# Optimization experiments

Measured on AMD Instinct MI355X. Metric: run time of the kernel, lower is better.

The kernel has to match this reference:

```python
import jax, jax.numpy as jnp
import numpy as np

B, SQ, SK, D, UNITS = 4, 2048, 2048, 1024, 1024

def setup_inputs() -> dict:
    key = jax.random.key(0)
    ks = jax.random.split(key, 5)
    scale = 1.0 / np.sqrt(D)
    return {
        "q": jax.random.normal(ks[0], (B, SQ, D), dtype=jnp.float32),
        "k": jax.random.normal(ks[1], (B, SK, D), dtype=jnp.float32),
        "v": jax.random.normal(ks[2], (B, SK, D), dtype=jnp.float32),
        "W1_w": jax.random.normal(ks[3], (D, UNITS), dtype=jnp.float32) * scale,
        "W1_b": jnp.zeros((UNITS,), dtype=jnp.float32),
        "W2_w": jax.random.normal(ks[4], (D, UNITS), dtype=jnp.float32) * scale,
        "W2_b": jnp.zeros((UNITS,), dtype=jnp.float32),
    }

def reference(q, k, v, W1_w, W1_b, W2_w, W2_b):
    # Dense projections (keras Dense: x @ W + b)
    l1 = q @ W1_w + W1_b            # [B, Sq, units]
    l2 = k @ W2_w + W2_b            # [B, Sk, units]
    # score = l1 @ l2^T, scaled by sqrt(score.shape[2]) == sqrt(Sk) (as in original)
    inv_scale = 1.0 / np.sqrt(k.shape[1]).astype(np.float32)
    score = jnp.einsum('bqu,bku->bqk', l1, l2) * inv_scale  # [B, Sq, Sk]
    dist = jax.nn.softmax(score, axis=-1)
    att = jnp.einsum('bqk,bkd->bqd', dist, v)               # [B, Sq, d_v]
    return att
```

## Files before the change

### kernel.cpp

```cpp
#include <hip/hip_runtime.h>
#include <cmath>
#include <stdint.h>


typedef short short8 __attribute__((ext_vector_type(8)));
typedef float f32x4 __attribute__((ext_vector_type(4)));
typedef __bf16 bf16x8 __attribute__((ext_vector_type(8)));

typedef __attribute__((address_space(3))) void lds_void;
typedef __attribute__((address_space(1))) void gbl_void;

__device__ __forceinline__ unsigned short f2b(float x) {
    unsigned u = __builtin_bit_cast(unsigned, x);
    u += 0x7fffu + ((u >> 16) & 1u);
    return (unsigned short)(u >> 16);
}

__global__ void prep_kernel(const float* __restrict__ q,
                            const float* __restrict__ k,
                            const float* __restrict__ v,
                            const float* __restrict__ W1,
                            const float* __restrict__ W2,
                            unsigned short* __restrict__ qbf,
                            unsigned short* __restrict__ kbf,
                            unsigned short* __restrict__ vT,
                            unsigned short* __restrict__ W1t,
                            unsigned short* __restrict__ W2t,
                            float* __restrict__ rs) {
    const int bz = blockIdx.z;
    const int t = threadIdx.x;

    if (bz >= 6) {
        const float* in = (bz < 8) ? q : k;
        unsigned short* out = (bz < 8) ? qbf : kbf;
        const long zi = (bz - 6) & 1;
        const long fb = zi * 2048 + blockIdx.y * 64 + blockIdx.x;
        const long i = (fb * 256 + t) * 8;
        float4 a = *(const float4*)(in + i);
        float4 b = *(const float4*)(in + i + 4);
        union { short8 v8; unsigned short u[8]; } r;
        r.u[0] = f2b(a.x); r.u[1] = f2b(a.y); r.u[2] = f2b(a.z); r.u[3] = f2b(a.w);
        r.u[4] = f2b(b.x); r.u[5] = f2b(b.y); r.u[6] = f2b(b.z); r.u[7] = f2b(b.w);
        *(short8*)(out + i) = r.v8;
        return;
    }

    const int tid2 = blockIdx.y * 64 + blockIdx.x;

    if (bz == 4 && tid2 >= 256 && tid2 < 288) {
        if (rs) rs[(tid2 - 256) * 256 + t] = 0.f;
        return;
    }

    __shared__ float tile[64][65];
    const float* in;
    unsigned short* out;
    int R, C;
    if (bz < 4) {
        R = 2048; C = 1024;
        if (tid2 >= 512) return;
        in = v + (long)bz * R * C;
        out = vT + (long)bz * R * C;
    } else {
        R = 1024; C = 1024;
        if (tid2 >= 256) return;
        in = (bz == 4) ? W1 : W2;
        out = (bz == 4) ? W1t : W2t;
    }
    const int rt = (tid2 >> 4) * 64;
    const int ct = (tid2 & 15) * 64;

    {
        const int rr = t >> 2;
        const int cb = (t & 3) * 16;
        const float* src = in + (long)(rt + rr) * C + ct + cb;
#pragma unroll
        for (int u = 0; u < 4; u++) {
            float4 a = *(const float4*)(src + 4 * u);
            tile[rr][cb + 4 * u + 0] = a.x;
            tile[rr][cb + 4 * u + 1] = a.y;
            tile[rr][cb + 4 * u + 2] = a.z;
            tile[rr][cb + 4 * u + 3] = a.w;
        }
    }
    __syncthreads();
    {
        const int cc = t >> 2;
        const int rb = (t & 3) * 16;
        unsigned short* dst = out + (long)(ct + cc) * R + rt + rb;
#pragma unroll
        for (int u = 0; u < 2; u++) {
            union { short8 v8; unsigned short us[8]; } o;
#pragma unroll
            for (int e = 0; e < 8; e++) o.us[e] = f2b(tile[rb + 8 * u + e][cc]);
            *(short8*)(dst + 8 * u) = o.v8;
        }
    }
}

__device__ __forceinline__ void load16_to_lds(const unsigned short* g,
                                              unsigned short* l) {
    __builtin_amdgcn_global_load_lds((gbl_void*)g, (lds_void*)l, 16, 0, 0);
}

template <int MODE>
__global__ __launch_bounds__(512, 4) void gemm256_kernel(
                               const unsigned short* __restrict__ A,
                               const unsigned short* __restrict__ Bt,
                               const float* __restrict__ bias0,
                               const float* __restrict__ bias1,
                               float* __restrict__ rowsum,
                               void* __restrict__ Cout,
                               int M, int N, int K,
                               float scale,
                               long sA, long sB, long sC) {
    __shared__ __align__(16) unsigned short As[256 * 64];
    __shared__ __align__(16) unsigned short Bs[128 * 64];

    int bx, by, bz;
    {
        const int nx = gridDim.x;
        const int Rt = gridDim.y * gridDim.z;
        if ((Rt & 7) == 0) {
            int flat = ((int)blockIdx.z * gridDim.y + blockIdx.y) * nx + blockIdx.x;
            int rpx = Rt >> 3;
            int c = flat & 7;
            int j = flat >> 3;
            bx = j / rpx;
            int yg = c * rpx + (j - bx * rpx);
            bz = yg / gridDim.y;
            by = yg - bz * gridDim.y;
        } else {
            bx = blockIdx.x; by = blockIdx.y; bz = blockIdx.z;
        }
    }

    A  += (long)bz * sA;
    Bt += (long)bz * sB;

    const int t = threadIdx.x;
    const int lane = t & 63;
    const int wave = t >> 6;
    const int wm = wave >> 1, wn = wave & 1;
    const int row0 = by * 256;
    const int col0 = bx * 128;

    const int rS = lane >> 3;
    const int kOffS = ((lane & 7) ^ rS) * 8;
    const unsigned short* gA[4];
    unsigned short* lA[4];
    const unsigned short* gB[2];
    unsigned short* lB[2];
#pragma unroll
    for (int i = 0; i < 4; i++) {
        const int rowl = wave * 32 + i * 8;
        gA[i] = A + (long)(row0 + rowl + rS) * K + kOffS;
        lA[i] = As + rowl * 64;
    }
#pragma unroll
    for (int i = 0; i < 2; i++) {
        const int rowl = wave * 16 + i * 8;
        gB[i] = Bt + (long)(col0 + rowl + rS) * K + kOffS;
        lB[i] = Bs + rowl * 64;
    }

    const int lr = lane & 15;
    const int quad = lane >> 4;
    const int pc0 = (quad ^ (lr & 7)) * 8;
    const int pc1 = ((4 + quad) ^ (lr & 7)) * 8;

    f32x4 acc[4][4];
#pragma unroll
    for (int i = 0; i < 4; i++)
#pragma unroll
        for (int j = 0; j < 4; j++) acc[i][j] = f32x4{0.f, 0.f, 0.f, 0.f};

    for (int k0 = 0; k0 < K; k0 += 64) {
#pragma unroll
        for (int i = 0; i < 4; i++) load16_to_lds(gA[i] + k0, lA[i]);
#pragma unroll
        for (int i = 0; i < 2; i++) load16_to_lds(gB[i] + k0, lB[i]);
        __syncthreads();

#pragma unroll
        for (int ks = 0; ks < 2; ks++) {
            const int pc = ks ? pc1 : pc0;
            bf16x8 a[4], b[4];
#pragma unroll
            for (int i = 0; i < 4; i++) {
                a[i] = __builtin_bit_cast(bf16x8,
                    *(const short8*)(As + (wm * 64 + i * 16 + lr) * 64 + pc));
                b[i] = __builtin_bit_cast(bf16x8,
                    *(const short8*)(Bs + (wn * 64 + i * 16 + lr) * 64 + pc));
            }
#pragma unroll
            for (int i = 0; i < 4; i++)
#pragma unroll
                for (int j = 0; j < 4; j++)
                    acc[i][j] = __builtin_amdgcn_mfma_f32_16x16x32_bf16(
                        a[i], b[j], acc[i][j], 0, 0, 0);
        }
        __syncthreads();
    }

    const long cbase = (long)bz * sC;

    if (MODE == 0) {
        const float* bp = (bz && bias1) ? bias1 : bias0;
#pragma unroll
        for (int j = 0; j < 4; j++) {
            const int gcol = col0 + wn * 64 + j * 16 + lr;
            const float bv = bp[gcol];
#pragma unroll
            for (int i = 0; i < 4; i++) {
                const int growb = row0 + wm * 64 + i * 16 + quad * 4;
#pragma unroll
                for (int r = 0; r < 4; r++) {
                    float val = acc[i][j][r] * scale + bv;
                    ((unsigned short*)Cout)[cbase + (long)(growb + r) * N + gcol] = f2b(val);
                }
            }
        }
    } else if (MODE == 1) {
        float psum[4][4];
#pragma unroll
        for (int i = 0; i < 4; i++)
#pragma unroll
            for (int r = 0; r < 4; r++) psum[i][r] = 0.f;
#pragma unroll
        for (int j = 0; j < 4; j++) {
            const int gcol = col0 + wn * 64 + j * 16 + lr;
#pragma unroll
            for (int i = 0; i < 4; i++) {
                const int growb = row0 + wm * 64 + i * 16 + quad * 4;
#pragma unroll
                for (int r = 0; r < 4; r++) {
                    float e = __expf(acc[i][j][r] * scale);
                    psum[i][r] += e;
                    ((unsigned short*)Cout)[cbase + (long)(growb + r) * N + gcol] = f2b(e);
                }
            }
        }
#pragma unroll
        for (int i = 0; i < 4; i++)
#pragma unroll
            for (int r = 0; r < 4; r++) {
                float s = psum[i][r];
                s += __shfl_xor(s, 1);
                s += __shfl_xor(s, 2);
                s += __shfl_xor(s, 4);
                s += __shfl_xor(s, 8);
                if (lr == 0) {
                    const int grow = row0 + wm * 64 + i * 16 + quad * 4 + r;
                    atomicAdd(rowsum + (long)bz * M + grow, s);
                }
            }
    } else {
#pragma unroll
        for (int i = 0; i < 4; i++) {
            const int growb = row0 + wm * 64 + i * 16 + quad * 4;
#pragma unroll
            for (int r = 0; r < 4; r++) {
                const float inv = 1.0f / rowsum[(long)bz * M + growb + r];
#pragma unroll
                for (int j = 0; j < 4; j++) {
                    const int gcol = col0 + wn * 64 + j * 16 + lr;
                    ((float*)Cout)[cbase + (long)(growb + r) * N + gcol] =
                        acc[i][j][r] * inv;
                }
            }
        }
    }
}

template <int MODE>
__global__ void gemm128_kernel(const unsigned short* __restrict__ A,
                               const unsigned short* __restrict__ Bt,
                               const float* __restrict__ bias0,
                               const float* __restrict__ bias1,
                               float* __restrict__ rowsum,
                               void* __restrict__ Cout,
                               int M, int N, int K,
                               float scale,
                               long sA, long sB, long sC) {
    __shared__ __align__(16) unsigned short As[128 * 64];
    __shared__ __align__(16) unsigned short Bs[128 * 64];

    int bx, by, bz;
    {
        const int nx = gridDim.x;
        const int Rt = gridDim.y * gridDim.z;
        if ((Rt & 7) == 0) {
            int flat = ((int)blockIdx.z * gridDim.y + blockIdx.y) * nx + blockIdx.x;
            int rpx = Rt >> 3;
            int c = flat & 7;
            int j = flat >> 3;
            bx = j / rpx;
            int yg = c * rpx + (j - bx * rpx);
            bz = yg / gridDim.y;
            by = yg - bz * gridDim.y;
        } else {
            bx = blockIdx.x; by = blockIdx.y; bz = blockIdx.z;
        }
    }

    A  += (long)bz * sA;
    Bt += (long)bz * sB;

    const int t = threadIdx.x;
    const int lane = t & 63;
    const int wave = t >> 6;
    const int wm = wave >> 1, wn = wave & 1;
    const int row0 = by * 128;
    const int col0 = bx * 128;

    const int rS = lane >> 3;
    const int kOffS = ((lane & 7) ^ rS) * 8;
    const unsigned short* gA[4];
    const unsigned short* gB[4];
    unsigned short* lA[4];
    unsigned short* lB[4];
#pragma unroll
    for (int i = 0; i < 4; i++) {
        const int rowl = i * 32 + wave * 8 + rS;
        const int ldsrow = i * 32 + wave * 8;
        gA[i] = A  + (long)(row0 + rowl) * K + kOffS;
        gB[i] = Bt + (long)(col0 + rowl) * K + kOffS;
        lA[i] = As + ldsrow * 64;
        lB[i] = Bs + ldsrow * 64;
    }

    const int lr = lane & 15;
    const int quad = lane >> 4;
    const int pc0 = (quad ^ (lr & 7)) * 8;
    const int pc1 = ((4 + quad) ^ (lr & 7)) * 8;

    f32x4 acc[4][4];
#pragma unroll
    for (int i = 0; i < 4; i++)
#pragma unroll
        for (int j = 0; j < 4; j++) acc[i][j] = f32x4{0.f, 0.f, 0.f, 0.f};

    for (int k0 = 0; k0 < K; k0 += 64) {
#pragma unroll
        for (int i = 0; i < 4; i++) {
            load16_to_lds(gA[i] + k0, lA[i]);
            load16_to_lds(gB[i] + k0, lB[i]);
        }
        __syncthreads();

#pragma unroll
        for (int ks = 0; ks < 2; ks++) {
            const int pc = ks ? pc1 : pc0;
            bf16x8 a[4], b[4];
#pragma unroll
            for (int i = 0; i < 4; i++) {
                a[i] = __builtin_bit_cast(bf16x8,
                    *(const short8*)(As + (wm * 64 + i * 16 + lr) * 64 + pc));
                b[i] = __builtin_bit_cast(bf16x8,
                    *(const short8*)(Bs + (wn * 64 + i * 16 + lr) * 64 + pc));
            }
#pragma unroll
            for (int i = 0; i < 4; i++)
#pragma unroll
                for (int j = 0; j < 4; j++)
                    acc[i][j] = __builtin_amdgcn_mfma_f32_16x16x32_bf16(
                        a[i], b[j], acc[i][j], 0, 0, 0);
        }
        __syncthreads();
    }

    const long cbase = (long)bz * sC;

    if (MODE == 0) {
        const float* bp = (bz && bias1) ? bias1 : bias0;
#pragma unroll
        for (int j = 0; j < 4; j++) {
            const int gcol = col0 + wn * 64 + j * 16 + lr;
            const float bv = bp[gcol];
#pragma unroll
            for (int i = 0; i < 4; i++) {
                const int growb = row0 + wm * 64 + i * 16 + quad * 4;
#pragma unroll
                for (int r = 0; r < 4; r++) {
                    float val = acc[i][j][r] * scale + bv;
                    ((unsigned short*)Cout)[cbase + (long)(growb + r) * N + gcol] = f2b(val);
                }
            }
        }
    } else if (MODE == 1) {
        float psum[4][4];
#pragma unroll
        for (int i = 0; i < 4; i++)
#pragma unroll
            for (int r = 0; r < 4; r++) psum[i][r] = 0.f;
#pragma unroll
        for (int j = 0; j < 4; j++) {
            const int gcol = col0 + wn * 64 + j * 16 + lr;
#pragma unroll
            for (int i = 0; i < 4; i++) {
                const int growb = row0 + wm * 64 + i * 16 + quad * 4;
#pragma unroll
                for (int r = 0; r < 4; r++) {
                    float e = __expf(acc[i][j][r] * scale);
                    psum[i][r] += e;
                    ((unsigned short*)Cout)[cbase + (long)(growb + r) * N + gcol] = f2b(e);
                }
            }
        }
#pragma unroll
        for (int i = 0; i < 4; i++)
#pragma unroll
            for (int r = 0; r < 4; r++) {
                float s = psum[i][r];
                s += __shfl_xor(s, 1);
                s += __shfl_xor(s, 2);
                s += __shfl_xor(s, 4);
                s += __shfl_xor(s, 8);
                if (lr == 0) {
                    const int grow = row0 + wm * 64 + i * 16 + quad * 4 + r;
                    atomicAdd(rowsum + (long)bz * M + grow, s);
                }
            }
    } else {
#pragma unroll
        for (int i = 0; i < 4; i++) {
            const int growb = row0 + wm * 64 + i * 16 + quad * 4;
#pragma unroll
            for (int r = 0; r < 4; r++) {
                const float inv = 1.0f / rowsum[(long)bz * M + growb + r];
#pragma unroll
                for (int j = 0; j < 4; j++) {
                    const int gcol = col0 + wn * 64 + j * 16 + lr;
                    ((float*)Cout)[cbase + (long)(growb + r) * N + gcol] =
                        acc[i][j][r] * inv;
                }
            }
        }
    }
}

extern "C" void kernel_launch(void* const* d_in, const int* in_sizes, int n_in,
                              void* d_out, int out_size, void* d_ws, size_t ws_size,
                              hipStream_t stream) {
    const float* q   = (const float*)d_in[0];
    const float* k   = (const float*)d_in[1];
    const float* v   = (const float*)d_in[2];
    const float* W1w = (const float*)d_in[3];
    const float* W1b = (const float*)d_in[4];
    const float* W2w = (const float*)d_in[5];
    const float* W2b = (const float*)d_in[6];
    float* out = (float*)d_out;

    const int B = 4, SQ = 2048, SK = 2048, D = 1024, U = 1024;
    char* ws = (char*)d_ws;
    const size_t MB = 1024 * 1024;
    unsigned short* qbf = (unsigned short*)(ws + 0);
    unsigned short* kbf = (unsigned short*)(ws + 16 * MB);
    unsigned short* vT  = (unsigned short*)(ws + 32 * MB);
    unsigned short* W1t = (unsigned short*)(ws + 48 * MB);
    unsigned short* W2t = (unsigned short*)(ws + 50 * MB);
    unsigned short* l1  = (unsigned short*)(ws + 52 * MB);
    unsigned short* l2  = (unsigned short*)(ws + 68 * MB);
    unsigned short* sc  = (unsigned short*)(ws + 0);

    float* rowsum;
    bool prep_zeroes_rowsum;
    if (ws_size >= 85 * MB) {
        rowsum = (float*)(ws + 84 * MB);
        prep_zeroes_rowsum = true;
    } else {
        rowsum = (float*)(ws + 50 * MB);
        prep_zeroes_rowsum = false;
    }

    prep_kernel<<<dim3(64, 32, 10), 256, 0, stream>>>(
        q, k, v, W1w, W2w, qbf, kbf, vT, W1t, W2t,
        prep_zeroes_rowsum ? rowsum : nullptr);
    gemm256_kernel<0><<<dim3(U / 128, (B * SQ) / 256, 2), 512, 0, stream>>>(
        qbf, W1t, W1b, W2b, nullptr, l1, B * SQ, U, D, 1.0f,
        (long)8 * 1024 * 1024, (long)1024 * 1024, (long)8 * 1024 * 1024);
    if (!prep_zeroes_rowsum)
        hipMemsetAsync(rowsum, 0, (size_t)B * SQ * sizeof(float), stream);
    const float invs = 1.0f / sqrtf((float)SK);
    gemm256_kernel<1><<<dim3(SK / 128, SQ / 256, B), 512, 0, stream>>>(
        l1, l2, nullptr, nullptr, rowsum, sc, SQ, SK, U, invs,
        (long)SQ * U, (long)SK * U, (long)SQ * SK);
    gemm128_kernel<2><<<dim3(D / 128, SQ / 128, B), 256, 0, stream>>>(
        sc, vT, nullptr, nullptr, rowsum, out, SQ, D, SK, 1.0f,
        (long)SQ * SK, (long)D * SK, (long)SQ * D);
}
```

Baseline: 265.5 us.

## Fuse fp32-to-bf16 cast of q and k into projection GEMM A-loads

Removes the separate prep pass that converted q and k to bf16 in workspace. The projection GEMM now reads fp32 q/k directly, converts them with v_cvt_pk_bf16_f32 and writes them into LDS through registers. This saves a full write and re-read of the bf16 copies. In exchange, the A operand no longer uses async global_load_lds, so it costs registers and may expose load latency in the unpipelined k-loop. Dead MODE branches are also pruned from both GEMM templates.

```diff
diff --git a/kernel.cpp b/kernel.cpp
--- a/kernel.cpp
+++ b/kernel.cpp
@@ -6,6 +6,7 @@
 typedef short short8 __attribute__((ext_vector_type(8)));
 typedef float f32x4 __attribute__((ext_vector_type(4)));
 typedef __bf16 bf16x8 __attribute__((ext_vector_type(8)));
+typedef unsigned int u32x4 __attribute__((ext_vector_type(4)));
 
 typedef __attribute__((address_space(3))) void lds_void;
 typedef __attribute__((address_space(1))) void gbl_void;
@@ -16,35 +17,15 @@
     return (unsigned short)(u >> 16);
 }
 
-__global__ void prep_kernel(const float* __restrict__ q,
-                            const float* __restrict__ k,
-                            const float* __restrict__ v,
+__global__ void prep_kernel(const float* __restrict__ v,
                             const float* __restrict__ W1,
                             const float* __restrict__ W2,
-                            unsigned short* __restrict__ qbf,
-                            unsigned short* __restrict__ kbf,
                             unsigned short* __restrict__ vT,
                             unsigned short* __restrict__ W1t,
                             unsigned short* __restrict__ W2t,
                             float* __restrict__ rs) {
     const int bz = blockIdx.z;
     const int t = threadIdx.x;
-
-    if (bz >= 6) {
-        const float* in = (bz < 8) ? q : k;
-        unsigned short* out = (bz < 8) ? qbf : kbf;
-        const long zi = (bz - 6) & 1;
-        const long fb = zi * 2048 + blockIdx.y * 64 + blockIdx.x;
-        const long i = (fb * 256 + t) * 8;
-        float4 a = *(const float4*)(in + i);
-        float4 b = *(const float4*)(in + i + 4);
-        union { short8 v8; unsigned short u[8]; } r;
-        r.u[0] = f2b(a.x); r.u[1] = f2b(a.y); r.u[2] = f2b(a.z); r.u[3] = f2b(a.w);
-        r.u[4] = f2b(b.x); r.u[5] = f2b(b.y); r.u[6] = f2b(b.z); r.u[7] = f2b(b.w);
-        *(short8*)(out + i) = r.v8;
-        return;
-    }
-
     const int tid2 = blockIdx.y * 64 + blockIdx.x;
 
     if (bz == 4 && tid2 >= 256 && tid2 < 288) {
@@ -58,7 +39,6 @@
     int R, C;
     if (bz < 4) {
         R = 2048; C = 1024;
-        if (tid2 >= 512) return;
         in = v + (long)bz * R * C;
         out = vT + (long)bz * R * C;
     } else {
@@ -103,7 +83,7 @@
     __builtin_amdgcn_global_load_lds((gbl_void*)g, (lds_void*)l, 16, 0, 0);
 }
 
-template <int MODE>
+template <int MODE, int CASTA>
 __global__ __launch_bounds__(512, 4) void gemm256_kernel(
                                const unsigned short* __restrict__ A,
                                const unsigned short* __restrict__ Bt,
@@ -113,7 +93,9 @@
                                void* __restrict__ Cout,
                                int M, int N, int K,
                                float scale,
-                               long sA, long sB, long sC) {
+                               long sA, long sB, long sC,
+                               const float* __restrict__ Afq,
+                               const float* __restrict__ Afk) {
     __shared__ __align__(16) unsigned short As[256 * 64];
     __shared__ __align__(16) unsigned short Bs[128 * 64];
 
@@ -135,7 +117,6 @@
         }
     }
 
-    A  += (long)bz * sA;
     Bt += (long)bz * sB;
 
     const int t = threadIdx.x;
@@ -148,14 +129,20 @@
     const int rS = lane >> 3;
     const int kOffS = ((lane & 7) ^ rS) * 8;
     const unsigned short* gA[4];
+    const float* fA[4];
     unsigned short* lA[4];
     const unsigned short* gB[2];
     unsigned short* lB[2];
 #pragma unroll
     for (int i = 0; i < 4; i++) {
         const int rowl = wave * 32 + i * 8;
-        gA[i] = A + (long)(row0 + rowl + rS) * K + kOffS;
         lA[i] = As + rowl * 64;
+        if (CASTA) {
+            const float* Af = bz ? Afk : Afq;
+            fA[i] = Af + (long)(row0 + rowl + rS) * K + kOffS;
+        } else {
+            gA[i] = A + (long)bz * sA + (long)(row0 + rowl + rS) * K + kOffS;
+        }
     }
 #pragma unroll
     for (int i = 0; i < 2; i++) {
@@ -177,9 +164,24 @@
 
     for (int k0 = 0; k0 < K; k0 += 64) {
 #pragma unroll
-        for (int i = 0; i < 4; i++) load16_to_lds(gA[i] + k0, lA[i]);
-#pragma unroll
         for (int i = 0; i < 2; i++) load16_to_lds(gB[i] + k0, lB[i]);
+        if (CASTA) {
+#pragma unroll
+            for (int i = 0; i < 4; i++) {
+                const float* s = fA[i] + k0;
+                float4 x = *(const float4*)(s);
+                float4 y = *(const float4*)(s + 4);
+                unsigned w0, w1, w2, w3;
+                asm("v_cvt_pk_bf16_f32 %0, %1, %2" : "=v"(w0) : "v"(x.x), "v"(x.y));
+                asm("v_cvt_pk_bf16_f32 %0, %1, %2" : "=v"(w1) : "v"(x.z), "v"(x.w));
+                asm("v_cvt_pk_bf16_f32 %0, %1, %2" : "=v"(w2) : "v"(y.x), "v"(y.y));
+                asm("v_cvt_pk_bf16_f32 %0, %1, %2" : "=v"(w3) : "v"(y.z), "v"(y.w));
+                *(u32x4*)(lA[i] + lane * 8) = u32x4{w0, w1, w2, w3};
+            }
+        } else {
+#pragma unroll
+            for (int i = 0; i < 4; i++) load16_to_lds(gA[i] + k0, lA[i]);
+        }
         __syncthreads();
 
 #pragma unroll
@@ -221,7 +223,7 @@
                 }
             }
         }
-    } else if (MODE == 1) {
+    } else {
         float psum[4][4];
 #pragma unroll
         for (int i = 0; i < 4; i++)
@@ -255,21 +257,6 @@
                     atomicAdd(rowsum + (long)bz * M + grow, s);
                 }
             }
-    } else {
-#pragma unroll
-        for (int i = 0; i < 4; i++) {
-            const int growb = row0 + wm * 64 + i * 16 + quad * 4;
-#pragma unroll
-            for (int r = 0; r < 4; r++) {
-                const float inv = 1.0f / rowsum[(long)bz * M + growb + r];
-#pragma unroll
-                for (int j = 0; j < 4; j++) {
-                    const int gcol = col0 + wn * 64 + j * 16 + lr;
-                    ((float*)Cout)[cbase + (long)(growb + r) * N + gcol] =
-                        acc[i][j][r] * inv;
-                }
-            }
-        }
     }
 }
 
@@ -372,57 +359,7 @@
 
     const long cbase = (long)bz * sC;
 
-    if (MODE == 0) {
-        const float* bp = (bz && bias1) ? bias1 : bias0;
-#pragma unroll
-        for (int j = 0; j < 4; j++) {
-            const int gcol = col0 + wn * 64 + j * 16 + lr;
-            const float bv = bp[gcol];
-#pragma unroll
-            for (int i = 0; i < 4; i++) {
-                const int growb = row0 + wm * 64 + i * 16 + quad * 4;
-#pragma unroll
-                for (int r = 0; r < 4; r++) {
-                    float val = acc[i][j][r] * scale + bv;
-                    ((unsigned short*)Cout)[cbase + (long)(growb + r) * N + gcol] = f2b(val);
-                }
-            }
-        }
-    } else if (MODE == 1) {
-        float psum[4][4];
-#pragma unroll
-        for (int i = 0; i < 4; i++)
-#pragma unroll
-            for (int r = 0; r < 4; r++) psum[i][r] = 0.f;
-#pragma unroll
-        for (int j = 0; j < 4; j++) {
-            const int gcol = col0 + wn * 64 + j * 16 + lr;
-#pragma unroll
-            for (int i = 0; i < 4; i++) {
-                const int growb = row0 + wm * 64 + i * 16 + quad * 4;
-#pragma unroll
-                for (int r = 0; r < 4; r++) {
-                    float e = __expf(acc[i][j][r] * scale);
-                    psum[i][r] += e;
-                    ((unsigned short*)Cout)[cbase + (long)(growb + r) * N + gcol] = f2b(e);
-                }
-            }
-        }
-#pragma unroll
-        for (int i = 0; i < 4; i++)
-#pragma unroll
-            for (int r = 0; r < 4; r++) {
-                float s = psum[i][r];
-                s += __shfl_xor(s, 1);
-                s += __shfl_xor(s, 2);
-                s += __shfl_xor(s, 4);
-                s += __shfl_xor(s, 8);
-                if (lr == 0) {
-                    const int grow = row0 + wm * 64 + i * 16 + quad * 4 + r;
-                    atomicAdd(rowsum + (long)bz * M + grow, s);
-                }
-            }
-    } else {
+    if (MODE == 2) {
 #pragma unroll
         for (int i = 0; i < 4; i++) {
             const int growb = row0 + wm * 64 + i * 16 + quad * 4;
@@ -455,8 +392,6 @@
     const int B = 4, SQ = 2048, SK = 2048, D = 1024, U = 1024;
     char* ws = (char*)d_ws;
     const size_t MB = 1024 * 1024;
-    unsigned short* qbf = (unsigned short*)(ws + 0);
-    unsigned short* kbf = (unsigned short*)(ws + 16 * MB);
     unsigned short* vT  = (unsigned short*)(ws + 32 * MB);
     unsigned short* W1t = (unsigned short*)(ws + 48 * MB);
     unsigned short* W2t = (unsigned short*)(ws + 50 * MB);
@@ -474,18 +409,18 @@
         prep_zeroes_rowsum = false;
     }
 
-    prep_kernel<<<dim3(64, 32, 10), 256, 0, stream>>>(
-        q, k, v, W1w, W2w, qbf, kbf, vT, W1t, W2t,
+    prep_kernel<<<dim3(64, 8, 6), 256, 0, stream>>>(
+        v, W1w, W2w, vT, W1t, W2t,
         prep_zeroes_rowsum ? rowsum : nullptr);
-    gemm256_kernel<0><<<dim3(U / 128, (B * SQ) / 256, 2), 512, 0, stream>>>(
-        qbf, W1t, W1b, W2b, nullptr, l1, B * SQ, U, D, 1.0f,
-        (long)8 * 1024 * 1024, (long)1024 * 1024, (long)8 * 1024 * 1024);
+    gemm256_kernel<0, 1><<<dim3(U / 128, (B * SQ) / 256, 2), 512, 0, stream>>>(
+        nullptr, W1t, W1b, W2b, nullptr, l1, B * SQ, U, D, 1.0f,
+        0, (long)1024 * 1024, (long)8 * 1024 * 1024, q, k);
     if (!prep_zeroes_rowsum)
         hipMemsetAsync(rowsum, 0, (size_t)B * SQ * sizeof(float), stream);
     const float invs = 1.0f / sqrtf((float)SK);
-    gemm256_kernel<1><<<dim3(SK / 128, SQ / 256, B), 512, 0, stream>>>(
+    gemm256_kernel<1, 0><<<dim3(SK / 128, SQ / 256, B), 512, 0, stream>>>(
         l1, l2, nullptr, nullptr, rowsum, sc, SQ, SK, U, invs,
-        (long)SQ * U, (long)SK * U, (long)SQ * SK);
+        (long)SQ * U, (long)SK * U, (long)SQ * SK, nullptr, nullptr);
     gemm128_kernel<2><<<dim3(D / 128, SQ / 128, B), 256, 0, stream>>>(
         sc, vT, nullptr, nullptr, rowsum, out, SQ, D, SK, 1.0f,
         (long)SQ * SK, (long)D * SK, (long)SQ * D);
```

Result: no change. 261.7 us (-1.4%).

## Fuse prep and three GEMMs into one cooperative persistent kernel with grid syncs

Applied to the files above, without the earlier changes.

Adds a cooperative mega_kernel of 512 blocks of 512 threads. It runs the bf16 casts, the transposes (now converting to bf16 inside LDS), the projection GEMM, the exp-score GEMM and the attention GEMM as phases separated by grid-wide syncs. Each phase is remapped so exactly 512 tiles fill the grid, and the final GEMM uses a new 8-wave 128x128 tile routine. The aim is to remove kernel launch boundaries and tail gaps between stages. In exchange it adds grid-barrier cost, fixes occupancy at the cooperative grid size, and keeps the old multi-kernel path as a fallback.

```diff
diff --git a/kernel.cpp b/kernel.cpp
--- a/kernel.cpp
+++ b/kernel.cpp
@@ -1,7 +1,10 @@
 #include <hip/hip_runtime.h>
+#include <hip/hip_cooperative_groups.h>
 #include <cmath>
 #include <stdint.h>
 
+
+namespace cg = cooperative_groups;
 
 typedef short short8 __attribute__((ext_vector_type(8)));
 typedef float f32x4 __attribute__((ext_vector_type(4)));
@@ -14,6 +17,349 @@
     unsigned u = __builtin_bit_cast(unsigned, x);
     u += 0x7fffu + ((u >> 16) & 1u);
     return (unsigned short)(u >> 16);
+}
+
+__device__ __forceinline__ void load16_to_lds(const unsigned short* g,
+                                              unsigned short* l) {
+    __builtin_amdgcn_global_load_lds((gbl_void*)g, (lds_void*)l, 16, 0, 0);
+}
+
+template <int MODE>
+__device__ __forceinline__ void gemm256_phase(
+        unsigned short* As, unsigned short* Bs,
+        const unsigned short* A, const unsigned short* Bt,
+        const float* bias0, const float* bias1,
+        float* rowsum, void* Cout,
+        int M, int N, int K, float scale,
+        long sA, long sB, long sC,
+        int bx, int by, int bz, int t) {
+    A  += (long)bz * sA;
+    Bt += (long)bz * sB;
+
+    const int lane = t & 63;
+    const int wave = t >> 6;
+    const int wm = wave >> 1, wn = wave & 1;
+    const int row0 = by * 256;
+    const int col0 = bx * 128;
+
+    const int rS = lane >> 3;
+    const int kOffS = ((lane & 7) ^ rS) * 8;
+    const unsigned short* gA[4];
+    unsigned short* lA[4];
+    const unsigned short* gB[2];
+    unsigned short* lB[2];
+#pragma unroll
+    for (int i = 0; i < 4; i++) {
+        const int rowl = wave * 32 + i * 8;
+        gA[i] = A + (long)(row0 + rowl + rS) * K + kOffS;
+        lA[i] = As + rowl * 64;
+    }
+#pragma unroll
+    for (int i = 0; i < 2; i++) {
+        const int rowl = wave * 16 + i * 8;
+        gB[i] = Bt + (long)(col0 + rowl + rS) * K + kOffS;
+        lB[i] = Bs + rowl * 64;
+    }
+
+    const int lr = lane & 15;
+    const int quad = lane >> 4;
+    const int pc0 = (quad ^ (lr & 7)) * 8;
+    const int pc1 = ((4 + quad) ^ (lr & 7)) * 8;
+
+    f32x4 acc[4][4];
+#pragma unroll
+    for (int i = 0; i < 4; i++)
+#pragma unroll
+        for (int j = 0; j < 4; j++) acc[i][j] = f32x4{0.f, 0.f, 0.f, 0.f};
+
+    for (int k0 = 0; k0 < K; k0 += 64) {
+#pragma unroll
+        for (int i = 0; i < 4; i++) load16_to_lds(gA[i] + k0, lA[i]);
+#pragma unroll
+        for (int i = 0; i < 2; i++) load16_to_lds(gB[i] + k0, lB[i]);
+        __syncthreads();
+
+#pragma unroll
+        for (int ks = 0; ks < 2; ks++) {
+            const int pc = ks ? pc1 : pc0;
+            bf16x8 a[4], b[4];
+#pragma unroll
+            for (int i = 0; i < 4; i++) {
+                a[i] = __builtin_bit_cast(bf16x8,
+                    *(const short8*)(As + (wm * 64 + i * 16 + lr) * 64 + pc));
+                b[i] = __builtin_bit_cast(bf16x8,
+                    *(const short8*)(Bs + (wn * 64 + i * 16 + lr) * 64 + pc));
+            }
+#pragma unroll
+            for (int i = 0; i < 4; i++)
+#pragma unroll
+                for (int j = 0; j < 4; j++)
+                    acc[i][j] = __builtin_amdgcn_mfma_f32_16x16x32_bf16(
+                        a[i], b[j], acc[i][j], 0, 0, 0);
+        }
+        __syncthreads();
+    }
+
+    const long cbase = (long)bz * sC;
+
+    if (MODE == 0) {
+        const float* bp = (bz && bias1) ? bias1 : bias0;
+#pragma unroll
+        for (int j = 0; j < 4; j++) {
+            const int gcol = col0 + wn * 64 + j * 16 + lr;
+            const float bv = bp[gcol];
+#pragma unroll
+            for (int i = 0; i < 4; i++) {
+                const int growb = row0 + wm * 64 + i * 16 + quad * 4;
+#pragma unroll
+                for (int r = 0; r < 4; r++) {
+                    float val = acc[i][j][r] * scale + bv;
+                    ((unsigned short*)Cout)[cbase + (long)(growb + r) * N + gcol] = f2b(val);
+                }
+            }
+        }
+    } else {
+        float psum[4][4];
+#pragma unroll
+        for (int i = 0; i < 4; i++)
+#pragma unroll
+            for (int r = 0; r < 4; r++) psum[i][r] = 0.f;
+#pragma unroll
+        for (int j = 0; j < 4; j++) {
+            const int gcol = col0 + wn * 64 + j * 16 + lr;
+#pragma unroll
+            for (int i = 0; i < 4; i++) {
+                const int growb = row0 + wm * 64 + i * 16 + quad * 4;
+#pragma unroll
+                for (int r = 0; r < 4; r++) {
+                    float e = __expf(acc[i][j][r] * scale);
+                    psum[i][r] += e;
+                    ((unsigned short*)Cout)[cbase + (long)(growb + r) * N + gcol] = f2b(e);
+                }
+            }
+        }
+#pragma unroll
+        for (int i = 0; i < 4; i++)
+#pragma unroll
+            for (int r = 0; r < 4; r++) {
+                float s = psum[i][r];
+                s += __shfl_xor(s, 1);
+                s += __shfl_xor(s, 2);
+                s += __shfl_xor(s, 4);
+                s += __shfl_xor(s, 8);
+                if (lr == 0) {
+                    const int grow = row0 + wm * 64 + i * 16 + quad * 4 + r;
+                    atomicAdd(rowsum + (long)bz * M + grow, s);
+                }
+            }
+    }
+}
+
+__device__ __forceinline__ void att512_phase(
+        unsigned short* As, unsigned short* Bs,
+        const unsigned short* A, const unsigned short* Bt,
+        const float* rowsum, float* out,
+        int bx, int by, int bz, int t) {
+    const int M = 2048, N = 1024, K = 2048;
+    const long sA = (long)M * K, sB = (long)N * K, sC = (long)M * N;
+    const unsigned short* Ab  = A  + (long)bz * sA;
+    const unsigned short* Btb = Bt + (long)bz * sB;
+
+    const int lane = t & 63;
+    const int w = t >> 6;
+    const int wm = w >> 1, wn = w & 1;
+    const int row0 = by * 128;
+    const int col0 = bx * 128;
+
+    const int rS = lane >> 3;
+    const int kOffS = ((lane & 7) ^ rS) * 8;
+    const unsigned short* gA[2];
+    unsigned short* lA[2];
+    const unsigned short* gB[2];
+    unsigned short* lB[2];
+#pragma unroll
+    for (int i = 0; i < 2; i++) {
+        const int rowl = w * 16 + i * 8;
+        gA[i] = Ab  + (long)(row0 + rowl + rS) * K + kOffS;
+        lA[i] = As + rowl * 64;
+        gB[i] = Btb + (long)(col0 + rowl + rS) * K + kOffS;
+        lB[i] = Bs + rowl * 64;
+    }
+
+    const int lr = lane & 15;
+    const int quad = lane >> 4;
+    const int pc0 = (quad ^ (lr & 7)) * 8;
+    const int pc1 = ((4 + quad) ^ (lr & 7)) * 8;
+
+    f32x4 acc[2][4];
+#pragma unroll
+    for (int i = 0; i < 2; i++)
+#pragma unroll
+        for (int j = 0; j < 4; j++) acc[i][j] = f32x4{0.f, 0.f, 0.f, 0.f};
+
+    for (int k0 = 0; k0 < K; k0 += 64) {
+#pragma unroll
+        for (int i = 0; i < 2; i++) {
+            load16_to_lds(gA[i] + k0, lA[i]);
+            load16_to_lds(gB[i] + k0, lB[i]);
+        }
+        __syncthreads();
+#pragma unroll
+        for (int ks = 0; ks < 2; ks++) {
+            const int pc = ks ? pc1 : pc0;
+            bf16x8 a[2], b[4];
+#pragma unroll
+            for (int i = 0; i < 2; i++)
+                a[i] = __builtin_bit_cast(bf16x8,
+                    *(const short8*)(As + (wm * 32 + i * 16 + lr) * 64 + pc));
+#pragma unroll
+            for (int j = 0; j < 4; j++)
+                b[j] = __builtin_bit_cast(bf16x8,
+                    *(const short8*)(Bs + (wn * 64 + j * 16 + lr) * 64 + pc));
+#pragma unroll
+            for (int i = 0; i < 2; i++)
+#pragma unroll
+                for (int j = 0; j < 4; j++)
+                    acc[i][j] = __builtin_amdgcn_mfma_f32_16x16x32_bf16(
+                        a[i], b[j], acc[i][j], 0, 0, 0);
+        }
+        __syncthreads();
+    }
+
+    const long cbase = (long)bz * sC;
+#pragma unroll
+    for (int i = 0; i < 2; i++) {
+        const int growb = row0 + wm * 32 + i * 16 + quad * 4;
+#pragma unroll
+        for (int r = 0; r < 4; r++) {
+            const float inv = 1.0f / rowsum[(long)bz * M + growb + r];
+#pragma unroll
+            for (int j = 0; j < 4; j++) {
+                const int gcol = col0 + wn * 64 + j * 16 + lr;
+                out[cbase + (long)(growb + r) * N + gcol] = acc[i][j][r] * inv;
+            }
+        }
+    }
+}
+
+struct MegaArgs {
+    const float *q, *k, *v, *W1, *W2, *b1, *b2;
+    unsigned short *qbf, *kbf, *vT, *W1t, *W2t, *l1, *l2, *sc;
+    float *rowsum, *out;
+    float invs;
+};
+
+__global__ __launch_bounds__(512, 4) void mega_kernel(MegaArgs a) {
+    __shared__ __align__(16) unsigned short As[256 * 64];
+    __shared__ __align__(16) unsigned short Bs[128 * 64];
+
+    const int bid = blockIdx.x;
+    const int t = threadIdx.x;
+    const int swz = (bid & 7) * 64 + (bid >> 3);
+
+#pragma unroll
+    for (int it = 0; it < 4; ++it) {
+        const long i = ((long)(it * 512 + bid) * 512 + t) * 8;
+        float4 x = *(const float4*)(a.q + i);
+        float4 y = *(const float4*)(a.q + i + 4);
+        union { short8 v8; unsigned short u[8]; } r;
+        r.u[0] = f2b(x.x); r.u[1] = f2b(x.y); r.u[2] = f2b(x.z); r.u[3] = f2b(x.w);
+        r.u[4] = f2b(y.x); r.u[5] = f2b(y.y); r.u[6] = f2b(y.z); r.u[7] = f2b(y.w);
+        *(short8*)(a.qbf + i) = r.v8;
+    }
+#pragma unroll
+    for (int it = 0; it < 4; ++it) {
+        const long i = ((long)(it * 512 + bid) * 512 + t) * 8;
+        float4 x = *(const float4*)(a.k + i);
+        float4 y = *(const float4*)(a.k + i + 4);
+        union { short8 v8; unsigned short u[8]; } r;
+        r.u[0] = f2b(x.x); r.u[1] = f2b(x.y); r.u[2] = f2b(x.z); r.u[3] = f2b(x.w);
+        r.u[4] = f2b(y.x); r.u[5] = f2b(y.y); r.u[6] = f2b(y.z); r.u[7] = f2b(y.w);
+        *(short8*)(a.kbf + i) = r.v8;
+    }
+    if (bid < 16) a.rowsum[bid * 512 + t] = 0.f;
+
+    {
+        const int half = t >> 8, st = t & 255;
+        unsigned short* tile = As + half * 8192;
+        for (int p = 0; p < 3; ++p) {
+            __syncthreads();
+            const int id = p * 1024 + bid * 2 + half;
+            const float* in = nullptr;
+            unsigned short* outp = nullptr;
+            int R = 0, C = 0, rt = 0, ct = 0;
+            bool active = false;
+            if (id < 2048) {
+                const int batch = id >> 9, ti = id & 511;
+                in = a.v + (long)batch * 2048 * 1024;
+                outp = a.vT + (long)batch * 1024 * 2048;
+                R = 2048; C = 1024;
+                rt = (ti >> 4) * 64; ct = (ti & 15) * 64;
+                active = true;
+            } else {
+                const int wdx = id - 2048;
+                if (wdx < 512) {
+                    in = (wdx < 256) ? a.W1 : a.W2;
+                    outp = (wdx < 256) ? a.W1t : a.W2t;
+                    const int ti = wdx & 255;
+                    R = 1024; C = 1024;
+                    rt = (ti >> 4) * 64; ct = (ti & 15) * 64;
+                    active = true;
+                }
+            }
+            if (active) {
+                const int rr = st >> 2, cb = (st & 3) * 16;
+                const float* src = in + (long)(rt + rr) * C + ct + cb;
+                unsigned short* trow = tile + rr * 65 + cb;
+#pragma unroll
+                for (int u = 0; u < 4; u++) {
+                    float4 x = *(const float4*)(src + 4 * u);
+                    trow[4 * u + 0] = f2b(x.x);
+                    trow[4 * u + 1] = f2b(x.y);
+                    trow[4 * u + 2] = f2b(x.z);
+                    trow[4 * u + 3] = f2b(x.w);
+                }
+            }
+            __syncthreads();
+            if (active) {
+                const int cc = st >> 2, rb = (st & 3) * 16;
+                unsigned short* dst = outp + (long)(ct + cc) * R + rt + rb;
+#pragma unroll
+                for (int u = 0; u < 2; u++) {
+                    union { short8 v8; unsigned short us[8]; } o;
+#pragma unroll
+                    for (int e = 0; e < 8; e++)
+                        o.us[e] = tile[(rb + 8 * u + e) * 65 + cc];
+                    *(short8*)(dst + 8 * u) = o.v8;
+                }
+            }
+        }
+    }
+
+    cg::this_grid().sync();
+
+    {
+        const int bx = swz & 7, by = (swz >> 3) & 31, bz = swz >> 8;
+        gemm256_phase<0>(As, Bs, a.qbf, a.W1t, a.b1, a.b2, nullptr, a.l1,
+                         8192, 1024, 1024, 1.0f,
+                         (long)8 * 1024 * 1024, (long)1024 * 1024,
+                         (long)8 * 1024 * 1024, bx, by, bz, t);
+    }
+    cg::this_grid().sync();
+
+    {
+        const int bx = swz & 15, by = (swz >> 4) & 7, bz = swz >> 7;
+        gemm256_phase<1>(As, Bs, a.l1, a.l2, nullptr, nullptr, a.rowsum, a.sc,
+                         2048, 2048, 1024, a.invs,
+                         (long)2048 * 1024, (long)2048 * 1024,
+                         (long)2048 * 2048, bx, by, bz, t);
+    }
+    cg::this_grid().sync();
+
+    {
+        const int bx = swz & 7, by = (swz >> 3) & 15, bz = swz >> 7;
+        att512_phase(As, Bs, a.sc, a.vT, a.rowsum, a.out, bx, by, bz, t);
+    }
 }
 
 __global__ void prep_kernel(const float* __restrict__ q,
@@ -46,7 +392,6 @@
     }
 
     const int tid2 = blockIdx.y * 64 + blockIdx.x;
-
     if (bz == 4 && tid2 >= 256 && tid2 < 288) {
         if (rs) rs[(tid2 - 256) * 256 + t] = 0.f;
         return;
@@ -69,24 +414,21 @@
     }
     const int rt = (tid2 >> 4) * 64;
     const int ct = (tid2 & 15) * 64;
-
-    {
-        const int rr = t >> 2;
-        const int cb = (t & 3) * 16;
+    {
+        const int rr = t >> 2, cb = (t & 3) * 16;
         const float* src = in + (long)(rt + rr) * C + ct + cb;
 #pragma unroll
         for (int u = 0; u < 4; u++) {
-            float4 a = *(const float4*)(src + 4 * u);
-            tile[rr][cb + 4 * u + 0] = a.x;
-            tile[rr][cb + 4 * u + 1] = a.y;
-            tile[rr][cb + 4 * u + 2] = a.z;
-            tile[rr][cb + 4 * u + 3] = a.w;
+            float4 x = *(const float4*)(src + 4 * u);
+            tile[rr][cb + 4 * u + 0] = x.x;
+            tile[rr][cb + 4 * u + 1] = x.y;
+            tile[rr][cb + 4 * u + 2] = x.z;
+            tile[rr][cb + 4 * u + 3] = x.w;
         }
     }
     __syncthreads();
     {
-        const int cc = t >> 2;
-        const int rb = (t & 3) * 16;
+        const int cc = t >> 2, rb = (t & 3) * 16;
         unsigned short* dst = out + (long)(ct + cc) * R + rt + rb;
 #pragma unroll
         for (int u = 0; u < 2; u++) {
@@ -98,25 +440,16 @@
     }
 }
 
-__device__ __forceinline__ void load16_to_lds(const unsigned short* g,
-                                              unsigned short* l) {
-    __builtin_amdgcn_global_load_lds((gbl_void*)g, (lds_void*)l, 16, 0, 0);
-}
-
 template <int MODE>
 __global__ __launch_bounds__(512, 4) void gemm256_kernel(
-                               const unsigned short* __restrict__ A,
-                               const unsigned short* __restrict__ Bt,
-                               const float* __restrict__ bias0,
-                               const float* __restrict__ bias1,
-                               float* __restrict__ rowsum,
-                               void* __restrict__ Cout,
-                               int M, int N, int K,
-                               float scale,
+                               const unsigned short* A,
+                               const unsigned short* Bt,
+                               const float* bias0, const float* bias1,
+                               float* rowsum, void* Cout,
+                               int M, int N, int K, float scale,
                                long sA, long sB, long sC) {
     __shared__ __align__(16) unsigned short As[256 * 64];
     __shared__ __align__(16) unsigned short Bs[128 * 64];
-
     int bx, by, bz;
     {
         const int nx = gridDim.x;
@@ -134,158 +467,20 @@
             bx = blockIdx.x; by = blockIdx.y; bz = blockIdx.z;
         }
     }
-
-    A  += (long)bz * sA;
-    Bt += (long)bz * sB;
-
-    const int t = threadIdx.x;
-    const int lane = t & 63;
-    const int wave = t >> 6;
-    const int wm = wave >> 1, wn = wave & 1;
-    const int row0 = by * 256;
-    const int col0 = bx * 128;
-
-    const int rS = lane >> 3;
-    const int kOffS = ((lane & 7) ^ rS) * 8;
-    const unsigned short* gA[4];
-    unsigned short* lA[4];
-    const unsigned short* gB[2];
-    unsigned short* lB[2];
-#pragma unroll
-    for (int i = 0; i < 4; i++) {
-        const int rowl = wave * 32 + i * 8;
-        gA[i] = A + (long)(row0 + rowl + rS) * K + kOffS;
-        lA[i] = As + rowl * 64;
-    }
-#pragma unroll
-    for (int i = 0; i < 2; i++) {
-        const int rowl = wave * 16 + i * 8;
-        gB[i] = Bt + (long)(col0 + rowl + rS) * K + kOffS;
-        lB[i] = Bs + rowl * 64;
-    }
-
-    const int lr = lane & 15;
-    const int quad = lane >> 4;
-    const int pc0 = (quad ^ (lr & 7)) * 8;
-    const int pc1 = ((4 + quad) ^ (lr & 7)) * 8;
-
-    f32x4 acc[4][4];
-#pragma unroll
-    for (int i = 0; i < 4; i++)
-#pragma unroll
-        for (int j = 0; j < 4; j++) acc[i][j] = f32x4{0.f, 0.f, 0.f, 0.f};
-
-    for (int k0 = 0; k0 < K; k0 += 64) {
-#pragma unroll
-        for (int i = 0; i < 4; i++) load16_to_lds(gA[i] + k0, lA[i]);
-#pragma unroll
-        for (int i = 0; i < 2; i++) load16_to_lds(gB[i] + k0, lB[i]);
-        __syncthreads();
-
-#pragma unroll
-        for (int ks = 0; ks < 2; ks++) {
-            const int pc = ks ? pc1 : pc0;
-            bf16x8 a[4], b[4];
-#pragma unroll
-            for (int i = 0; i < 4; i++) {
-                a[i] = __builtin_bit_cast(bf16x8,
-                    *(const short8*)(As + (wm * 64 + i * 16 + lr) * 64 + pc));
-                b[i] = __builtin_bit_cast(bf16x8,
-                    *(const short8*)(Bs + (wn * 64 + i * 16 + lr) * 64 + pc));
-            }
-#pragma unroll
-            for (int i = 0; i < 4; i++)
-#pragma unroll
-                for (int j = 0; j < 4; j++)
-                    acc[i][j] = __builtin_amdgcn_mfma_f32_16x16x32_bf16(
-                        a[i], b[j], acc[i][j], 0, 0, 0);
-        }
-        __syncthreads();
-    }
-
-    const long cbase = (long)bz * sC;
-
-    if (MODE == 0) {
-        const float* bp = (bz && bias1) ? bias1 : bias0;
-#pragma unroll
-        for (int j = 0; j < 4; j++) {
-            const int gcol = col0 + wn * 64 + j * 16 + lr;
-            const float bv = bp[gcol];
-#pragma unroll
-            for (int i = 0; i < 4; i++) {
-                const int growb = row0 + wm * 64 + i * 16 + quad * 4;
-#pragma unroll
-                for (int r = 0; r < 4; r++) {
-                    float val = acc[i][j][r] * scale + bv;
-                    ((unsigned short*)Cout)[cbase + (long)(growb + r) * N + gcol] = f2b(val);
-                }
-            }
-        }
-    } else if (MODE == 1) {
-        float psum[4][4];
-#pragma unroll
-        for (int i = 0; i < 4; i++)
-#pragma unroll
-            for (int r = 0; r < 4; r++) psum[i][r] = 0.f;
-#pragma unroll
-        for (int j = 0; j < 4; j++) {
-            const int gcol = col0 + wn * 64 + j * 16 + lr;
-#pragma unroll
-            for (int i = 0; i < 4; i++) {
-                const int growb = row0 + wm * 64 + i * 16 + quad * 4;
-#pragma unroll
-                for (int r = 0; r < 4; r++) {
-                    float e = __expf(acc[i][j][r] * scale);
-                    psum[i][r] += e;
-                    ((unsigned short*)Cout)[cbase + (long)(growb + r) * N + gcol] = f2b(e);
-                }
-            }
-        }
-#pragma unroll
-        for (int i = 0; i < 4; i++)
-#pragma unroll
-            for (int r = 0; r < 4; r++) {
-                float s = psum[i][r];
-                s += __shfl_xor(s, 1);
-                s += __shfl_xor(s, 2);
-                s += __shfl_xor(s, 4);
-                s += __shfl_xor(s, 8);
-                if (lr == 0) {
-                    const int grow = row0 + wm * 64 + i * 16 + quad * 4 + r;
-                    atomicAdd(rowsum + (long)bz * M + grow, s);
-                }
-            }
-    } else {
-#pragma unroll
-        for (int i = 0; i < 4; i++) {
-            const int growb = row0 + wm * 64 + i * 16 + quad * 4;
-#pragma unroll
-            for (int r = 0; r < 4; r++) {
-                const float inv = 1.0f / rowsum[(long)bz * M + growb + r];
-#pragma unroll
-                for (int j = 0; j < 4; j++) {
-                    const int gcol = col0 + wn * 64 + j * 16 + lr;
-                    ((float*)Cout)[cbase + (long)(growb + r) * N + gcol] =
-                        acc[i][j][r] * inv;
-                }
-            }
-        }
-    }
+    gemm256_phase<MODE>(As, Bs, A, Bt, bias0, bias1, rowsum, Cout,
+                        M, N, K, scale, sA, sB, sC, bx, by, bz,
+                        (int)threadIdx.x);
 }
 
 template <int MODE>
 __global__ void gemm128_kernel(const unsigned short* __restrict__ A,
                                const unsigned short* __restrict__ Bt,
-                               const float* __restrict__ bias0,
-                               const float* __restrict__ bias1,
                                float* __restrict__ rowsum,
                                void* __restrict__ Cout,
                                int M, int N, int K,
-                               float scale,
                                long sA, long sB, long sC) {
     __shared__ __align__(16) unsigned short As[128 * 64];
     __shared__ __align__(16) unsigned short Bs[128 * 64];
-
     int bx, by, bz;
     {
         const int nx = gridDim.x;
@@ -306,7 +501,6 @@
 
     A  += (long)bz * sA;
     Bt += (long)bz * sB;
-
     const int t = threadIdx.x;
     const int lane = t & 63;
     const int wave = t >> 6;
@@ -329,7 +523,6 @@
         lA[i] = As + ldsrow * 64;
         lB[i] = Bs + ldsrow * 64;
     }
-
     const int lr = lane & 15;
     const int quad = lane >> 4;
     const int pc0 = (quad ^ (lr & 7)) * 8;
@@ -348,7 +541,6 @@
             load16_to_lds(gB[i] + k0, lB[i]);
         }
         __syncthreads();
-
 #pragma unroll
         for (int ks = 0; ks < 2; ks++) {
             const int pc = ks ? pc1 : pc0;
@@ -371,58 +563,7 @@
     }
 
     const long cbase = (long)bz * sC;
-
-    if (MODE == 0) {
-        const float* bp = (bz && bias1) ? bias1 : bias0;
-#pragma unroll
-        for (int j = 0; j < 4; j++) {
-            const int gcol = col0 + wn * 64 + j * 16 + lr;
-            const float bv = bp[gcol];
-#pragma unroll
-            for (int i = 0; i < 4; i++) {
-                const int growb = row0 + wm * 64 + i * 16 + quad * 4;
-#pragma unroll
-                for (int r = 0; r < 4; r++) {
-                    float val = acc[i][j][r] * scale + bv;
-                    ((unsigned short*)Cout)[cbase + (long)(growb + r) * N + gcol] = f2b(val);
-                }
-            }
-        }
-    } else if (MODE == 1) {
-        float psum[4][4];
-#pragma unroll
-        for (int i = 0; i < 4; i++)
-#pragma unroll
-            for (int r = 0; r < 4; r++) psum[i][r] = 0.f;
-#pragma unroll
-        for (int j = 0; j < 4; j++) {
-            const int gcol = col0 + wn * 64 + j * 16 + lr;
-#pragma unroll
-            for (int i = 0; i < 4; i++) {
-                const int growb = row0 + wm * 64 + i * 16 + quad * 4;
-#pragma unroll
-                for (int r = 0; r < 4; r++) {
-                    float e = __expf(acc[i][j][r] * scale);
-                    psum[i][r] += e;
-                    ((unsigned short*)Cout)[cbase + (long)(growb + r) * N + gcol] = f2b(e);
-                }
-            }
-        }
-#pragma unroll
-        for (int i = 0; i < 4; i++)
-#pragma unroll
-            for (int r = 0; r < 4; r++) {
-                float s = psum[i][r];
-                s += __shfl_xor(s, 1);
-                s += __shfl_xor(s, 2);
-                s += __shfl_xor(s, 4);
-                s += __shfl_xor(s, 8);
-                if (lr == 0) {
-                    const int grow = row0 + wm * 64 + i * 16 + quad * 4 + r;
-                    atomicAdd(rowsum + (long)bz * M + grow, s);
-                }
-            }
-    } else {
+    if (MODE == 2) {
 #pragma unroll
         for (int i = 0; i < 4; i++) {
             const int growb = row0 + wm * 64 + i * 16 + quad * 4;
@@ -463,6 +604,28 @@
     unsigned short* l1  = (unsigned short*)(ws + 52 * MB);
     unsigned short* l2  = (unsigned short*)(ws + 68 * MB);
     unsigned short* sc  = (unsigned short*)(ws + 0);
+    const float invs = 1.0f / sqrtf((float)SK);
+
+    static int coop_support = -1;
+    if (coop_support < 0) {
+        int dev = 0, val = 0;
+        (void)hipGetDevice(&dev);
+        if (hipDeviceGetAttribute(&val, hipDeviceAttributeCooperativeLaunch,
+                                  dev) != hipSuccess) val = 0;
+        coop_support = val;
+    }
+
+    if (coop_support && ws_size >= 85 * MB) {
+        float* rowsum = (float*)(ws + 84 * MB);
+        MegaArgs margs = { q, k, v, W1w, W2w, W1b, W2b,
+                           qbf, kbf, vT, W1t, W2t, l1, l2, sc,
+                           rowsum, out, invs };
+        void* kargs[] = { (void*)&margs };
+        hipError_t e = hipLaunchCooperativeKernel(
+            (const void*)mega_kernel, dim3(512), dim3(512), kargs, 0, stream);
+        if (e == hipSuccess) return;
+        (void)hipGetLastError();
+    }
 
     float* rowsum;
     bool prep_zeroes_rowsum;
@@ -482,11 +645,10 @@
         (long)8 * 1024 * 1024, (long)1024 * 1024, (long)8 * 1024 * 1024);
     if (!prep_zeroes_rowsum)
         hipMemsetAsync(rowsum, 0, (size_t)B * SQ * sizeof(float), stream);
-    const float invs = 1.0f / sqrtf((float)SK);
     gemm256_kernel<1><<<dim3(SK / 128, SQ / 256, B), 512, 0, stream>>>(
         l1, l2, nullptr, nullptr, rowsum, sc, SQ, SK, U, invs,
         (long)SQ * U, (long)SK * U, (long)SQ * SK);
     gemm128_kernel<2><<<dim3(D / 128, SQ / 128, B), 256, 0, stream>>>(
-        sc, vT, nullptr, nullptr, rowsum, out, SQ, D, SK, 1.0f,
+        sc, vT, rowsum, out, SQ, D, SK,
         (long)SQ * SK, (long)D * SK, (long)SQ * D);
 }
```

New measurement: 505.6 us. 90.4% more time.
